# Performance work log

Measured on AMD Instinct MI355X. Metric: run time of the kernel, lower is better.

## Reference

```python
import jax, jax.numpy as jnp
import numpy as np
import math

NEG = -10000.0  # module uses -10000, not -inf


def setup_inputs() -> dict:
    key = jax.random.key(0)
    k1, k2, k3 = jax.random.split(key, 3)
    B, Sq, Sk, H, Hkv, D = 2, 2048, 2048, 16, 4, 64
    q = jax.random.normal(k1, (B, Sq, H, D), dtype=jnp.float32)
    kv = jax.random.normal(k2, (B, Sk, 2, Hkv, D), dtype=jnp.float32)
    key_padding_mask = jax.random.randint(k3, (B, Sk), 0, 2) > 0  # True = valid key
    return {"q": q, "kv": kv, "key_padding_mask": key_padding_mask}


def reference(q, kv, key_padding_mask):
    B, Sq, H, D = q.shape
    Sk, Hkv = kv.shape[1], kv.shape[3]
    if Hkv != H:
        # einops repeat '... hkv d -> ... (hkv g) d': each kv head repeated g times contiguously
        kv = jnp.repeat(kv, H // Hkv, axis=3)
    k, v = kv[:, :, 0], kv[:, :, 1]  # [B, Sk, H, D] each
    scale = 1.0 / math.sqrt(D)
    scores = jnp.einsum('bthd,bshd->bhts', q, k * scale)  # [B, H, Sq, Sk]
    # key padding: additive 0 where valid, -10000 where padded
    pad = jnp.where(key_padding_mask, 0.0, NEG).astype(scores.dtype)
    scores = scores + pad[:, None, None, :]
    # causal mask: cols > rows + Sk - Sq gets replaced (not added) with -10000
    rows = jnp.arange(Sq)[:, None]
    cols = jnp.arange(Sk)[None, :]
    causal_mask = cols > rows + (Sk - Sq)
    scores = jnp.where(causal_mask, NEG, scores)
    attention = jax.nn.softmax(scores, axis=-1).astype(v.dtype)
    # dropout p=0.0 -> identity
    output = jnp.einsum('bhts,bshd->bthd', attention, v)  # [B, Sq, H, D]
    return output
```

## Files before the change

kernel.cpp:

```cpp
#include <hip/hip_runtime.h>
#include <math.h>


typedef __bf16 bf16x4 __attribute__((ext_vector_type(4)));
typedef __bf16 bf16x8 __attribute__((ext_vector_type(8)));
typedef float floatx4 __attribute__((ext_vector_type(4)));
typedef short shortx4 __attribute__((ext_vector_type(4)));

#define B_ 2
#define SQ 2048
#define SK 2048
#define H_ 16
#define HKV 4
#define D_ 64
#define QT 64
#define KT 64
#define PADLD 72
#define KVROW 512
#define NEGV (-10000.0f)
#define QSCL 0.18033688f
#define EBIAS 17.3123405f

static __device__ __forceinline__ floatx4 mfma16(bf16x4 a, bf16x4 b, floatx4 c) {
#if __has_builtin(__builtin_amdgcn_mfma_f32_16x16x16bf16_1k)
    return __builtin_amdgcn_mfma_f32_16x16x16bf16_1k(
        __builtin_bit_cast(shortx4, a), __builtin_bit_cast(shortx4, b), c, 0, 0, 0);
#else
    floatx4 d;
    asm("v_mfma_f32_16x16x16_bf16 %0, %1, %2, %3"
        : "=v"(d) : "v"(a), "v"(b), "v"(c));
    return d;
#endif
}

__global__ __launch_bounds__(256, 4)
void attn_kernel(const float* __restrict__ q,
                 const float* __restrict__ kv,
                 const int* __restrict__ mask,
                 float* __restrict__ out)
{
    __shared__ alignas(16) union {
        struct {
            __bf16 Kt[KT][PADLD];
            __bf16 Vt[D_][PADLD];
        } m;
        struct {
            float fpart[4][64];
            float fw[4][64];
            int   s_first;
        } f;
    } sh;

    const int tid  = threadIdx.x;
    const int wave = tid >> 6;
    const int lane = tid & 63;
    const int col  = lane & 15;
    const int quad = lane >> 4;

    if (blockIdx.x < 32) {
        const int bh = (int)blockIdx.x;
        const int b = bh >> 4, h = bh & 15, hkv = h >> 2;
        if (tid == 0) sh.f.s_first = SK;
        __syncthreads();
        int local = SK;
        for (int s = tid; s < SK; s += 256)
            if (mask[b * SK + s]) local = min(local, s);
        atomicMin(&sh.f.s_first, local);
        __syncthreads();
        const int nfirst = sh.f.s_first;
        if (nfirst == 0) return;

        const float* kvb = kv + (size_t)b * SK * KVROW + hkv * D_;
        const float* vvb = kvb + HKV * D_;
        {
            float a0=0,a1=0,a2=0,a3=0,a4=0,a5=0,a6=0,a7=0;
            const int s0 = wave * 512;
            for (int s = s0; s < s0 + 512; s += 8) {
                a0 += vvb[(size_t)(s+0)*KVROW + lane];
                a1 += vvb[(size_t)(s+1)*KVROW + lane];
                a2 += vvb[(size_t)(s+2)*KVROW + lane];
                a3 += vvb[(size_t)(s+3)*KVROW + lane];
                a4 += vvb[(size_t)(s+4)*KVROW + lane];
                a5 += vvb[(size_t)(s+5)*KVROW + lane];
                a6 += vvb[(size_t)(s+6)*KVROW + lane];
                a7 += vvb[(size_t)(s+7)*KVROW + lane];
            }
            sh.f.fpart[wave][lane] = ((a0+a1)+(a2+a3)) + ((a4+a5)+(a6+a7));
        }
        __syncthreads();
        const float vtotal = sh.f.fpart[0][lane] + sh.f.fpart[1][lane]
                           + sh.f.fpart[2][lane] + sh.f.fpart[3][lane];

        for (int R = wave; R < nfirst; R += 4) {
            const float* qrow = q + (((size_t)b * SQ + R) * H_ + h) * D_;
            float mymax = -3.4e38f;
            for (int s = lane; s <= R; s += 64) {
                const float* kp = kvb + (size_t)s * KVROW;
                float dt = 0.f;
                for (int d = 0; d < D_; ++d) dt += qrow[d] * kp[d];
                mymax = fmaxf(mymax, dt * 0.125f + NEGV);
            }
#pragma unroll
            for (int off = 32; off >= 1; off >>= 1)
                mymax = fmaxf(mymax, __shfl_xor(mymax, off, 64));
            const float M = (R < SK - 1) ? fmaxf(mymax, NEGV) : mymax;
            float lsum = 0.f, oacc = 0.f, pref = 0.f;
            for (int s0 = 0; s0 <= R; s0 += 64) {
                int s = s0 + lane;
                float w = 0.f;
                if (s <= R) {
                    const float* kp = kvb + (size_t)s * KVROW;
                    float dt = 0.f;
                    for (int d = 0; d < D_; ++d) dt += qrow[d] * kp[d];
                    w = __expf(dt * 0.125f + NEGV - M);
                    lsum += w;
                }
                sh.f.fw[wave][lane] = w;
                const int nk = (R - s0 + 1 < 64) ? (R - s0 + 1) : 64;
                for (int j = 0; j < nk; ++j) {
                    const float vj = vvb[(size_t)(s0 + j) * KVROW + lane];
                    oacc += sh.f.fw[wave][j] * vj;
                    pref += vj;
                }
            }
#pragma unroll
            for (int off = 32; off >= 1; off >>= 1)
                lsum += __shfl_xor(lsum, off, 64);
            const float wn   = __expf(NEGV - M);
            const float ltot = lsum + wn * (float)(SK - 1 - R);
            out[(((size_t)b * SQ + R) * H_ + h) * D_ + lane] =
                (oacc + wn * (vtotal - pref)) / ltot;
        }
        return;
    }

    const int id = (int)blockIdx.x - 32;
    const int bh = id & 31;
    const int y  = id >> 5;
    const int kg = y >> 3, jj = y & 7;
    const int qt = (kg == 0) ? 31 - jj : (kg == 1) ? jj : (kg == 2) ? 23 - jj : 8 + jj;
    const int b = bh >> 4, h = bh & 15, hkv = h >> 2;
    const int q0 = qt * QT;
    const int qw = q0 + wave * 16;

    bf16x8 aq[2];
    {
        const int row = qw + col;
        const float* qp = q + (((size_t)b * SQ + row) * H_ + h) * D_ + quad * 8;
#pragma unroll
        for (int kc = 0; kc < 2; ++kc) {
            const float* p = qp + kc * 32;
#pragma unroll
            for (int j = 0; j < 8; ++j) aq[kc][j] = (__bf16)(p[j] * QSCL);
        }
    }

    bf16x4 vone4;
#pragma unroll
    for (int j = 0; j < 4; ++j) vone4[j] = (__bf16)1.0f;

    floatx4 o[4];
    floatx4 l_acc = (floatx4){0.f, 0.f, 0.f, 0.f};
#pragma unroll
    for (int dj = 0; dj < 4; ++dj) o[dj] = (floatx4){0.f, 0.f, 0.f, 0.f};

    const int kkey = tid >> 4;
    const int kd   = (tid & 15) * 4;
    const int vkey = (tid & 15) * 4;
    const int vd   = (tid >> 4) * 4;

    const float* kvb = kv + (size_t)b * SK * KVROW + hkv * D_;

    float4 kreg[4], vreg[4];
    int mreg = 0;

    auto prefetch = [&](int kt) {
        const float* kb = kvb + (size_t)kt * KT * KVROW;
#pragma unroll
        for (int i = 0; i < 4; ++i)
            kreg[i] = *(const float4*)(kb + (kkey + 16 * i) * KVROW + kd);
        const float* vb = kb + HKV * D_;
#pragma unroll
        for (int i = 0; i < 4; ++i)
            vreg[i] = *(const float4*)(vb + (vkey + i) * KVROW + vd);
        mreg = mask[b * SK + kt * KT + lane];
    };

    auto stage = [&]() {
#pragma unroll
        for (int i = 0; i < 4; ++i) {
            bf16x4 t = { (__bf16)kreg[i].x, (__bf16)kreg[i].y,
                         (__bf16)kreg[i].z, (__bf16)kreg[i].w };
            *(bf16x4*)&sh.m.Kt[kkey + 16 * i][kd] = t;
        }
        const float* vf = (const float*)vreg;
#pragma unroll
        for (int j = 0; j < 4; ++j) {
            bf16x4 t = { (__bf16)vf[0*4+j], (__bf16)vf[1*4+j],
                         (__bf16)vf[2*4+j], (__bf16)vf[3*4+j] };
            *(bf16x4*)&sh.m.Vt[vd + j][vkey] = t;
        }
    };

    const int nkt = qt + 1;
    prefetch(0);

    for (int kt = 0; kt < nkt; ++kt) {
        stage();
        const unsigned long long kept = __ballot(mreg != 0);
        __syncthreads();
        if (kt + 1 < nkt) prefetch(kt + 1);

        floatx4 c[4];
#pragma unroll
        for (int kj = 0; kj < 4; ++kj) {
            c[kj] = (floatx4){0.f, 0.f, 0.f, 0.f};
#pragma unroll
            for (int kc = 0; kc < 2; ++kc) {
                bf16x8 ak = *(const bf16x8*)&sh.m.Kt[kj * 16 + col][kc * 32 + quad * 8];
                c[kj] = __builtin_amdgcn_mfma_f32_16x16x32_bf16(ak, aq[kc], c[kj], 0, 0, 0);
            }
        }

        const bool dg = (kt == qt);
        const unsigned long long kq = kept >> (quad * 4);
        const int tcl = dg ? (wave * 16 + col - quad * 4) : 127;
        bf16x4 pk[4];
#pragma unroll
        for (int kj = 0; kj < 4; ++kj) {
#pragma unroll
            for (int r = 0; r < 4; ++r) {
                float p = __builtin_amdgcn_exp2f(c[kj][r] - EBIAS);
                const bool keep = ((kq >> (kj * 16 + r)) & 1ull) && (kj * 16 + r <= tcl);
                pk[kj][r] = (__bf16)(keep ? p : 0.f);
            }
        }

#pragma unroll
        for (int kj = 0; kj < 4; ++kj)
            l_acc = mfma16(pk[kj], vone4, l_acc);

#pragma unroll
        for (int dj = 0; dj < 4; ++dj)
#pragma unroll
            for (int kj = 0; kj < 4; ++kj) {
                bf16x4 bv = *(const bf16x4*)&sh.m.Vt[dj * 16 + col][kj * 16 + quad * 4];
                o[dj] = mfma16(pk[kj], bv, o[dj]);
            }
        __syncthreads();
    }

#pragma unroll
    for (int r = 0; r < 4; ++r) {
        const float l = l_acc[r];
        if (l > 0.f) {
            const float inv = 1.0f / l;
            const int row = qw + quad * 4 + r;
            float* op = out + (((size_t)b * SQ + row) * H_ + h) * D_ + col;
#pragma unroll
            for (int dj = 0; dj < 4; ++dj)
                op[dj * 16] = o[dj][r] * inv;
        }
    }
}

extern "C" void kernel_launch(void* const* d_in, const int* in_sizes, int n_in,
                              void* d_out, int out_size, void* d_ws, size_t ws_size,
                              hipStream_t stream) {
    const float* q   = (const float*)d_in[0];
    const float* kv  = (const float*)d_in[1];
    const int* mask  = (const int*)d_in[2];
    float* out       = (float*)d_out;
    attn_kernel<<<dim3(32 + 1024), 256, 0, stream>>>(q, kv, mask, out);
}
```

Measured before the change: 123.0 us.

## Split long causal query tiles across key ranges and combine partial sums

Query tiles that cover many key tiles are split into chunks of up to 8 key tiles. Each chunk writes its unnormalized output and row sums to a workspace, and a second combine kernel sums the chunks and normalizes. This shortens the longest blocks and raises the block count, which evens out causal load imbalance. Launch bounds also move to 8 waves per SIMD. The cost is extra workspace traffic, a second launch, and possible register pressure from the tighter launch bounds.

```diff
diff --git a/kernel.cpp b/kernel.cpp
--- a/kernel.cpp
+++ b/kernel.cpp
@@ -20,6 +20,8 @@
 #define NEGV (-10000.0f)
 #define QSCL 0.18033688f
 #define EBIAS 17.3123405f
+#define SLOTF 4160
+#define SLOTS_PER_BH 72
 
 static __device__ __forceinline__ floatx4 mfma16(bf16x4 a, bf16x4 b, floatx4 c) {
 #if __has_builtin(__builtin_amdgcn_mfma_f32_16x16x16bf16_1k)
@@ -33,11 +35,12 @@
 #endif
 }
 
-__global__ __launch_bounds__(256, 4)
+__global__ __launch_bounds__(256, 8)
 void attn_kernel(const float* __restrict__ q,
                  const float* __restrict__ kv,
                  const int* __restrict__ mask,
-                 float* __restrict__ out)
+                 float* __restrict__ out,
+                 float* __restrict__ ws)
 {
     __shared__ alignas(16) union {
         struct {
@@ -136,9 +139,16 @@
 
     const int id = (int)blockIdx.x - 32;
     const int bh = id & 31;
-    const int y  = id >> 5;
-    const int kg = y >> 3, jj = y & 7;
-    const int qt = (kg == 0) ? 31 - jj : (kg == 1) ? jj : (kg == 2) ? 23 - jj : 8 + jj;
+    const int z  = 79 - (id >> 5);
+    int qt, sp;
+    if (z < 8)       { qt = z;                sp = 0; }
+    else if (z < 24) { qt = 8 + ((z - 8) >> 1);  sp = (z - 8) & 1; }
+    else if (z < 48) { qt = 16 + (z - 24) / 3;   sp = (z - 24) % 3; }
+    else             { qt = 24 + ((z - 48) >> 2); sp = (z - 48) & 3; }
+    const int nsplit = 1 + (qt >> 3);
+    const int k0 = sp * 8;
+    const int k1 = min(qt + 1, k0 + 8);
+
     const int b = bh >> 4, h = bh & 15, hkv = h >> 2;
     const int q0 = qt * QT;
     const int qw = q0 + wave * 16;
@@ -202,14 +212,13 @@
         }
     };
 
-    const int nkt = qt + 1;
-    prefetch(0);
-
-    for (int kt = 0; kt < nkt; ++kt) {
+    prefetch(k0);
+
+    for (int kt = k0; kt < k1; ++kt) {
         stage();
         const unsigned long long kept = __ballot(mreg != 0);
         __syncthreads();
-        if (kt + 1 < nkt) prefetch(kt + 1);
+        if (kt + 1 < k1) prefetch(kt + 1);
 
         floatx4 c[4];
 #pragma unroll
@@ -250,16 +259,71 @@
         __syncthreads();
     }
 
-#pragma unroll
-    for (int r = 0; r < 4; ++r) {
-        const float l = l_acc[r];
-        if (l > 0.f) {
-            const float inv = 1.0f / l;
-            const int row = qw + quad * 4 + r;
-            float* op = out + (((size_t)b * SQ + row) * H_ + h) * D_ + col;
+    if (nsplit == 1) {
+#pragma unroll
+        for (int r = 0; r < 4; ++r) {
+            const float l = l_acc[r];
+            if (l > 0.f) {
+                const float inv = 1.0f / l;
+                const int row = qw + quad * 4 + r;
+                float* op = out + (((size_t)b * SQ + row) * H_ + h) * D_ + col;
+#pragma unroll
+                for (int dj = 0; dj < 4; ++dj)
+                    op[dj * 16] = o[dj][r] * inv;
+            }
+        }
+    } else {
+        const int local0 = (qt < 16) ? (qt - 8) * 2
+                         : (qt < 24) ? 16 + (qt - 16) * 3
+                                     : 40 + (qt - 24) * 4;
+        float* slot = ws + ((size_t)bh * SLOTS_PER_BH + local0 + sp) * SLOTF;
+#pragma unroll
+        for (int r = 0; r < 4; ++r) {
+            const int row = wave * 16 + quad * 4 + r;
+            float* op = slot + (size_t)row * 64 + col;
 #pragma unroll
             for (int dj = 0; dj < 4; ++dj)
-                op[dj * 16] = o[dj][r] * inv;
+                op[dj * 16] = o[dj][r];
+            if (col == 0) slot[4096 + row] = l_acc[r];
+        }
+    }
+}
+
+__global__ __launch_bounds__(256)
+void combine_kernel(const float* __restrict__ ws, float* __restrict__ out)
+{
+    __shared__ float linv[64];
+    const int tid = threadIdx.x;
+    const int bh = (int)blockIdx.x & 31;
+    const int qt = 8 + ((int)blockIdx.x >> 5);
+    const int b = bh >> 4, h = bh & 15;
+    const int n = 1 + (qt >> 3);
+    const int local0 = (qt < 16) ? (qt - 8) * 2
+                     : (qt < 24) ? 16 + (qt - 16) * 3
+                                 : 40 + (qt - 24) * 4;
+    const float* s0 = ws + ((size_t)bh * SLOTS_PER_BH + local0) * SLOTF;
+
+    if (tid < 64) {
+        float s = 0.f;
+        for (int k = 0; k < n; ++k)
+            s += s0[(size_t)k * SLOTF + 4096 + tid];
+        linv[tid] = (s > 0.f) ? 1.0f / s : 0.f;
+    }
+    __syncthreads();
+
+#pragma unroll
+    for (int c = 0; c < 4; ++c) {
+        const int idx = c * 1024 + tid * 4;
+        const int row = idx >> 6, d = idx & 63;
+        float4 acc = *(const float4*)(s0 + idx);
+        for (int k = 1; k < n; ++k) {
+            const float4 t = *(const float4*)(s0 + (size_t)k * SLOTF + idx);
+            acc.x += t.x; acc.y += t.y; acc.z += t.z; acc.w += t.w;
+        }
+        const float inv = linv[row];
+        if (inv > 0.f) {
+            float4 r4 = { acc.x * inv, acc.y * inv, acc.z * inv, acc.w * inv };
+            *(float4*)(out + (((size_t)b * SQ + qt * 64 + row) * H_ + h) * D_ + d) = r4;
         }
     }
 }
@@ -271,5 +335,6 @@
     const float* kv  = (const float*)d_in[1];
     const int* mask  = (const int*)d_in[2];
     float* out       = (float*)d_out;
-    attn_kernel<<<dim3(32 + 1024), 256, 0, stream>>>(q, kv, mask, out);
+    attn_kernel<<<dim3(32 + 2560), 256, 0, stream>>>(q, kv, mask, out, (float*)d_ws);
+    combine_kernel<<<dim3(768), 256, 0, stream>>>((const float*)d_ws, out);
 }
```

Result: slower. 343.3 us (+179.1%).
